# Kernel optimization log

Hardware: AMD Instinct MI355X
Metric: run time of the kernel (lower is better)

## Reference

```python
import jax, jax.numpy as jnp
import numpy as np

T_SCALE = 160
NUM_SAMPLE = 32
FEAT_DIM = 2048
HIDDEN = 512
N_CLASS = 20
BATCH = 8


def build_sample_mask(tscale=T_SCALE, ns=NUM_SAMPLE):
    # Vectorized version of _get_interp1d_mask (prop_boundary_ratio=0, num_sample_perbin=1).
    # Returns mask of shape [tscale, ns, start, end] (already transposed as in the torch code).
    s = np.arange(tscale)[:, None, None]           # start
    e = np.arange(tscale)[None, :, None]           # end
    k = np.arange(ns)[None, None, :]
    pos = s + (e - s) * k / (ns - 1.0)             # [T, T, ns] sample positions
    Sg, Eg, Kg = np.broadcast_arrays(s, e, k)
    posf = pos.ravel(); Sf = Sg.ravel(); Ef = Eg.ravel(); Kf = Kg.ravel()
    valid = Ef >= Sf
    frac, dn = np.modf(posf)
    dn = dn.astype(np.int64)
    up = np.ceil(posf).astype(np.int64)
    mask = np.zeros((tscale, ns, tscale, tscale), dtype=np.float32)
    m1 = valid & (dn >= 0) & (dn <= tscale - 1)
    np.add.at(mask, (dn[m1], Kf[m1], Sf[m1], Ef[m1]), (1.0 - frac[m1]).astype(np.float32))
    m2 = valid & (up >= 0) & (up <= tscale - 1)
    np.add.at(mask, (up[m2], Kf[m2], Sf[m2], Ef[m2]), frac[m2].astype(np.float32))
    return jnp.asarray(mask)


def conv1d(x, w, padding):
    # x: [B, Cin, T], w: [Cout, Cin, K]
    return jax.lax.conv_general_dilated(
        x, w, window_strides=(1,), padding=[(padding, padding)],
        dimension_numbers=("NCH", "OIH", "NCH"))


def setup_inputs() -> dict:
    key = jax.random.key(0)
    ks = jax.random.split(key, 6)
    x = jax.random.normal(ks[0], (BATCH, T_SCALE, FEAT_DIM), dtype=jnp.float32)
    w1 = jax.random.normal(ks[1], (HIDDEN, FEAT_DIM, 3), dtype=jnp.float32) * 0.02
    b1 = jnp.zeros((HIDDEN,), dtype=jnp.float32)
    wc = jax.random.normal(ks[2], (N_CLASS, HIDDEN, 1), dtype=jnp.float32) * 0.05
    wa = jax.random.normal(ks[3], (1, HIDDEN, 3), dtype=jnp.float32) * 0.05
    ba = jnp.zeros((1,), dtype=jnp.float32)
    sample_mask = build_sample_mask()  # [T, ns, T, T]
    return {"x": x, "sample_mask": sample_mask, "w1": w1, "b1": b1,
            "wc": wc, "wa": wa, "ba": ba}


def reference(x, sample_mask, w1, b1, wc, wa, ba):
    ns = NUM_SAMPLE
    q = ns // 4  # 8
    xp = jnp.transpose(x, (0, 2, 1))                   # [B, F, T]
    feat = jax.nn.relu(conv1d(xp, w1, 1) + b1[None, :, None])   # [B, H, T] (dropout = eval/identity)
    y_class = conv1d(feat, wc, 0)                      # [B, C, T]
    y_atn = conv1d(feat, wa, 1) + ba[None, :, None]    # [B, 1, T]
    # boundary matching: matmul against sparse interpolation mask
    out = jnp.einsum("bct,tkij->bckij", y_class, sample_mask)   # [B, C, ns, T, T]
    out_start = out[:, :, :q].mean(axis=2)
    out_mid = out[:, :, q:ns - q].mean(axis=2)
    out_end = out[:, :, ns - q:].mean(axis=2)
    bmn_class = jnp.concatenate((out_start, out_mid, out_end), axis=1)  # [B, 3C, T, T]
    sig = jax.nn.sigmoid(y_atn)
    x_fg = (sig * feat).sum(-1, keepdims=True) / (sig.sum(-1, keepdims=True) + 1e-8)  # [B, H, 1]
    y_fg = jnp.einsum("oh,bht->bot", wc[:, :, 0], x_fg)  # conv_class 1x1, no bias
    return (y_class, y_fg, bmn_class)
```

## Files before the change

kernel.cpp:

```cpp
#include <hip/hip_runtime.h>
#include <math.h>

#define TS 160
#define FEATD 2048
#define HID 512
#define NC 20
#define NB 8

typedef __attribute__((ext_vector_type(8))) short bfrag;
typedef __attribute__((ext_vector_type(4))) float f32x4;

static __device__ __forceinline__ unsigned short f2bf(float f) {
  unsigned int u = __float_as_uint(f);
  unsigned int r = (u + 0x7FFFu + ((u >> 16) & 1u)) >> 16;
  return (unsigned short)r;
}
static __device__ __forceinline__ float bf2f(unsigned short s) {
  return __uint_as_float(((unsigned int)s) << 16);
}

static __device__ __forceinline__ void gload16(const void* g, void* l) {
  __builtin_amdgcn_global_load_lds((const __attribute__((address_space(1))) void*)g,
                                   (__attribute__((address_space(3))) void*)l, 16, 0, 0);
}

__global__ __launch_bounds__(256) void k_prep(const float* __restrict__ x,
                                              const float* __restrict__ w1,
                                              unsigned short* __restrict__ xb,
                                              unsigned short* __restrict__ wb,
                                              unsigned short* __restrict__ WT) {
  __shared__ float Ls[FEATD * 3];
  const int tid = threadIdx.x;
  const int bx = blockIdx.x;
  if (bx < 1296) {
    const int idx = bx * 256 + tid;
    const int c = (idx & 255) * 8;
    const int row = idx >> 8;
    const int b = row / 162, pr = row - b * 162;
    unsigned short* o = xb + (size_t)row * FEATD + c;
    if (pr == 0 || pr == 161) {
      *(uint4*)o = make_uint4(0u, 0u, 0u, 0u);
    } else {
      const float* src = x + ((size_t)(b * TS + pr - 1)) * FEATD + c;
      float4 v0 = *(const float4*)src;
      float4 v1 = *(const float4*)(src + 4);
      unsigned short r[8] = {f2bf(v0.x), f2bf(v0.y), f2bf(v0.z), f2bf(v0.w),
                             f2bf(v1.x), f2bf(v1.y), f2bf(v1.z), f2bf(v1.w)};
      *(uint4*)o = *(const uint4*)r;
    }
  } else if (bx < 1808) {
    const int h = bx - 1296;
    const float4* src = (const float4*)(w1 + (size_t)h * (FEATD * 3));
    for (int e = tid; e < FEATD * 3 / 4; e += 256) ((float4*)Ls)[e] = src[e];
    __syncthreads();
    for (int oc = tid; oc < 768; oc += 256) {
      const int tap = oc >> 8;
      const int f0 = (oc & 255) * 8;
      unsigned short r[8];
      #pragma unroll
      for (int i = 0; i < 8; ++i) r[i] = f2bf(Ls[(f0 + i) * 3 + tap]);
      *(uint4*)&wb[((size_t)tap * HID + h) * FEATD + f0] = *(const uint4*)r;
    }
  } else {
    const int idx = (bx - 1808) * 256 + tid;
    const int tau = idx % 160;
    const int dd = (idx / 160) % 320;
    const int g = idx / (160 * 320);
    float w = 0.f;
    if (dd >= 160) {
      const int d = dd - 160;
      const int k0 = (g == 0) ? 0 : (g == 1 ? 8 : 24);
      const int k1 = (g == 0) ? 8 : (g == 1 ? 24 : 32);
      for (int k = k0; k < k1; ++k) {
        float p = (float)(d * k) / 31.0f;
        float a = fabsf(p - (float)tau);
        w += fmaxf(0.f, 1.f - a);
      }
      w *= (g == 1) ? 0.0625f : 0.125f;
    }
    WT[idx] = f2bf(w);
  }
}

__global__ __launch_bounds__(256, 3) void k_conv_mfma(const unsigned short* __restrict__ xb,
                                                      const unsigned short* __restrict__ wb,
                                                      unsigned short* __restrict__ part) {
  const int bb = blockIdx.x;
  const int h0 = blockIdx.y * 64;
  const int kz = blockIdx.z;
  const int tid = threadIdx.x;
  const int wid = tid >> 6, lane = tid & 63;

  __shared__ unsigned short Alds[162 * 64];
  __shared__ unsigned short Blds[3 * 64 * 64];

  const unsigned short* xbb = xb + (size_t)bb * 162 * FEATD;
  const unsigned short* wbb = wb + (size_t)h0 * FEATD;

  f32x4 acc[5][2] = {};
  const int wr = wid >> 1, wc = wid & 1;

  for (int s = 0; s < 4; ++s) {
    const int f0 = kz * 256 + s * 64;
    #pragma unroll
    for (int is = 0; is < 5; ++is) {
      const int ci = is * 256 + wid * 64 + lane;
      const int row = ci >> 3, c = ci & 7;
      gload16(xbb + (size_t)row * FEATD + f0 + ((c ^ (row & 7)) << 3),
              (char*)Alds + (size_t)(is * 256 + wid * 64) * 16);
    }
    #pragma unroll
    for (int is = 0; is < 6; ++is) {
      const int ci = is * 256 + wid * 64 + lane;
      const int tap = ci >> 9, rr = (ci >> 3) & 63, c = ci & 7;
      gload16(wbb + (size_t)tap * (HID * FEATD) + (size_t)rr * FEATD + f0 + ((c ^ (rr & 7)) << 3),
              (char*)Blds + (size_t)(is * 256 + wid * 64) * 16);
    }
    if (tid < 16) {
      const int row = 160 + (tid >> 3), c = tid & 7;
      uint4 v = *(const uint4*)(xbb + (size_t)row * FEATD + f0 + ((c ^ (row & 7)) << 3));
      *(uint4*)((char*)Alds + row * 128 + c * 16) = v;
    }
    __syncthreads();

    #pragma unroll
    for (int tap = 0; tap < 3; ++tap) {
      #pragma unroll
      for (int kk = 0; kk < 2; ++kk) {
        const int cread = kk * 4 + (lane >> 4);
        bfrag bf0, bf1;
        {
          const int hh0 = wc * 32 + (lane & 15);
          const int hh1 = hh0 + 16;
          bf0 = *(const bfrag*)((char*)Blds + tap * 8192 + hh0 * 128 + ((cread ^ (hh0 & 7)) << 4));
          bf1 = *(const bfrag*)((char*)Blds + tap * 8192 + hh1 * 128 + ((cread ^ (hh1 & 7)) << 4));
        }
        #pragma unroll
        for (int mi = 0; mi < 5; ++mi) {
          const int rr = wr * 80 + mi * 16 + (lane & 15) + tap;
          bfrag af = *(const bfrag*)((char*)Alds + rr * 128 + ((cread ^ (rr & 7)) << 4));
          acc[mi][0] = __builtin_amdgcn_mfma_f32_16x16x32_bf16(af, bf0, acc[mi][0], 0, 0, 0);
          acc[mi][1] = __builtin_amdgcn_mfma_f32_16x16x32_bf16(af, bf1, acc[mi][1], 0, 0, 0);
        }
      }
    }
    __syncthreads();
  }

  unsigned short* pout = part + (size_t)kz * (NB * TS) * HID;
  #pragma unroll
  for (int mi = 0; mi < 5; ++mi) {
    const int r0 = bb * TS + wr * 80 + mi * 16 + (lane >> 4) * 4;
    #pragma unroll
    for (int ni = 0; ni < 2; ++ni) {
      const int c0 = h0 + wc * 32 + ni * 16 + (lane & 15);
      #pragma unroll
      for (int i = 0; i < 4; ++i)
        pout[(size_t)(r0 + i) * HID + c0] = f2bf(acc[mi][ni][i]);
    }
  }
}

__global__ __launch_bounds__(256) void k_bias_relu(const unsigned short* __restrict__ part,
                                                   const float* __restrict__ bias,
                                                   float* __restrict__ feat) {
  const int idx = blockIdx.x * 256 + threadIdx.x;
  const int h0 = (idx & 63) * 8;
  float a[8];
  {
    float4 b0 = *(const float4*)&bias[h0];
    float4 b1 = *(const float4*)&bias[h0 + 4];
    a[0] = b0.x; a[1] = b0.y; a[2] = b0.z; a[3] = b0.w;
    a[4] = b1.x; a[5] = b1.y; a[6] = b1.z; a[7] = b1.w;
  }
  #pragma unroll
  for (int kz = 0; kz < 8; ++kz) {
    uint4 v = *(const uint4*)&part[(size_t)kz * (NB * TS * HID) + (size_t)idx * 8];
    const unsigned short* s = (const unsigned short*)&v;
    #pragma unroll
    for (int k = 0; k < 8; ++k) a[k] += bf2f(s[k]);
  }
  float4 o0, o1;
  o0.x = fmaxf(a[0], 0.f); o0.y = fmaxf(a[1], 0.f); o0.z = fmaxf(a[2], 0.f); o0.w = fmaxf(a[3], 0.f);
  o1.x = fmaxf(a[4], 0.f); o1.y = fmaxf(a[5], 0.f); o1.z = fmaxf(a[6], 0.f); o1.w = fmaxf(a[7], 0.f);
  *(float4*)&feat[(size_t)idx * 8] = o0;
  *(float4*)&feat[(size_t)idx * 8 + 4] = o1;
}

__global__ __launch_bounds__(256) void k_head(const float* __restrict__ feat,
                                              const float* __restrict__ wc,
                                              const float* __restrict__ wa,
                                              const float* __restrict__ ba,
                                              float* __restrict__ y_class,
                                              float* __restrict__ y_atn) {
  __shared__ float wcs[NC * HID];
  __shared__ float was[HID * 3];
  const int tid = threadIdx.x;
  for (int e = tid; e < NC * HID; e += 256) wcs[e] = wc[e];
  for (int e = tid; e < HID * 3; e += 256) was[e] = wa[e];
  __syncthreads();
  const int wave = blockIdx.x * 4 + (tid >> 6);
  const int lane = tid & 63;
  const int b = wave / TS, t = wave - b * TS;
  const float* frow = &feat[((size_t)b * TS + t) * HID];
  float fc[8], fm[8], fp[8];
  #pragma unroll
  for (int i2 = 0; i2 < 8; ++i2) {
    int h = lane + 64 * i2;
    fc[i2] = frow[h];
    fm[i2] = (t > 0)      ? frow[h - HID] : 0.f;
    fp[i2] = (t < TS - 1) ? frow[h + HID] : 0.f;
  }
  #pragma unroll 4
  for (int c = 0; c < NC; ++c) {
    float p = 0.f;
    #pragma unroll
    for (int i2 = 0; i2 < 8; ++i2) p += fc[i2] * wcs[c * HID + lane + 64 * i2];
    #pragma unroll
    for (int off = 32; off; off >>= 1) p += __shfl_xor(p, off);
    if (lane == 0) y_class[((size_t)b * NC + c) * TS + t] = p;
  }
  float p = 0.f;
  #pragma unroll
  for (int i2 = 0; i2 < 8; ++i2) {
    int h = lane + 64 * i2;
    p += fm[i2] * was[h * 3 + 0] + fc[i2] * was[h * 3 + 1] + fp[i2] * was[h * 3 + 2];
  }
  #pragma unroll
  for (int off = 32; off; off >>= 1) p += __shfl_xor(p, off);
  if (lane == 0) y_atn[b * TS + t] = p + ba[0];
}

__global__ __launch_bounds__(256) void k_tail(const float* __restrict__ y_class,
                                              const unsigned short* __restrict__ WT,
                                              const float* __restrict__ feat,
                                              const float* __restrict__ y_atn,
                                              const float* __restrict__ wc,
                                              float* __restrict__ y_fg,
                                              float* __restrict__ bmn) {
  __shared__ char Tlds[64000 + 65536];
  const int tid = threadIdx.x;

  if (blockIdx.y == 3) {
    if (blockIdx.x >= 8) return;
    const int b = blockIdx.x;
    float* sig = (float*)Tlds;
    float* red = sig + TS;
    float* xfg = red + 8;
    float s = 0.f;
    if (tid < TS) { s = 1.f / (1.f + expf(-y_atn[b * TS + tid])); sig[tid] = s; }
    float r = s;
    #pragma unroll
    for (int off = 32; off; off >>= 1) r += __shfl_xor(r, off);
    if ((tid & 63) == 0) red[tid >> 6] = r;
    __syncthreads();
    const float inv = 1.f / (red[0] + red[1] + red[2] + red[3] + 1e-8f);
    for (int h = tid; h < HID; h += 256) {
      float a = 0.f;
      for (int t = 0; t < TS; ++t) a += sig[t] * feat[((size_t)b * TS + t) * HID + h];
      xfg[h] = a * inv;
    }
    __syncthreads();
    const int wv = tid >> 6, lane = tid & 63;
    for (int c = wv; c < NC; c += 4) {
      float p = 0.f;
      #pragma unroll
      for (int i2 = 0; i2 < 8; ++i2) {
        int h = lane + 64 * i2;
        p += wc[c * HID + h] * xfg[h];
      }
      #pragma unroll
      for (int off = 32; off; off >>= 1) p += __shfl_xor(p, off);
      if (lane == 0) y_fg[b * NC + c] = p;
    }
    return;
  }

  char* Alds = Tlds;
  char* Wlds = Tlds + 64000;
  const int i = blockIdx.x;
  const int g = blockIdx.y;
  const int wid = tid >> 6, lane = tid & 63;

  const char* wtb = (const char*)WT + (size_t)g * 102400 + (size_t)(160 - i) * 320;
  #pragma unroll
  for (int it = 0; it < 16; ++it) {
    const int idx = it * 256 + tid;
    int row = idx / 25, c = idx - row * 25;
    if (row > 159) row = 159;
    if (c > 19) c = 0;
    gload16(wtb + (size_t)row * 320 + c * 16, Wlds + (size_t)idx * 16);
  }
  for (int e = 0; e < 13; ++e) {
    const int ci = e * 256 + tid;
    if (ci < 3200) {
      const int row = ci / 20, c = ci - row * 20;
      const int tb = i + c * 8;
      const float* yr = y_class + (size_t)row * TS;
      unsigned short r8[8];
      #pragma unroll
      for (int k = 0; k < 8; ++k) {
        const int t = tb + k;
        r8[k] = (t < TS) ? f2bf(yr[t]) : (unsigned short)0;
      }
      *(uint4*)(Alds + (size_t)row * 400 + c * 16) = *(const uint4*)r8;
    }
  }
  __syncthreads();

  const int wr = wid >> 1, wcq = wid & 1;
  f32x4 acc[5][5] = {};

  #pragma unroll
  for (int ks = 0; ks < 5; ++ks) {
    const int cc = ks * 4 + (lane >> 4);
    bfrag bfr[5];
    #pragma unroll
    for (int nf = 0; nf < 5; ++nf) {
      const int j = wcq * 80 + nf * 16 + (lane & 15);
      bfr[nf] = *(const bfrag*)(Wlds + (size_t)j * 400 + cc * 16);
    }
    #pragma unroll
    for (int mf = 0; mf < 5; ++mf) {
      const int r = wr * 80 + mf * 16 + (lane & 15);
      bfrag af = *(const bfrag*)(Alds + (size_t)r * 400 + cc * 16);
      #pragma unroll
      for (int nf = 0; nf < 5; ++nf)
        acc[mf][nf] = __builtin_amdgcn_mfma_f32_16x16x32_bf16(af, bfr[nf], acc[mf][nf], 0, 0, 0);
    }
  }

  #pragma unroll
  for (int mf = 0; mf < 5; ++mf) {
    const int r0 = wr * 80 + mf * 16 + (lane >> 4) * 4;
    #pragma unroll
    for (int reg = 0; reg < 4; ++reg) {
      const int r = r0 + reg;
      const int b = r / 20, c = r - b * 20;
      float* base = bmn + (((size_t)(b * 60 + g * 20 + c) * TS) + i) * TS;
      #pragma unroll
      for (int nf = 0; nf < 5; ++nf) {
        const int j = wcq * 80 + nf * 16 + (lane & 15);
        base[j] = acc[mf][nf][reg];
      }
    }
  }
}

extern "C" void kernel_launch(void* const* d_in, const int* in_sizes, int n_in,
                              void* d_out, int out_size, void* d_ws, size_t ws_size,
                              hipStream_t stream) {
  const float* x  = (const float*)d_in[0];
  const float* w1 = (const float*)d_in[2];
  const float* b1 = (const float*)d_in[3];
  const float* wc = (const float*)d_in[4];
  const float* wa = (const float*)d_in[5];
  const float* ba = (const float*)d_in[6];

  float* out     = (float*)d_out;
  float* y_class = out;
  float* y_fg    = out + NB * NC * TS;
  float* bmn     = out + NB * NC * TS + NB * NC;

  unsigned short* part = (unsigned short*)d_ws;
  float* feat  = (float*)((char*)d_ws + (size_t)8 * NB * TS * HID * 2);
  float* y_atn = feat + NB * TS * HID;
  unsigned short* xb = (unsigned short*)(y_atn + 2048);
  unsigned short* wb = xb + (size_t)NB * 162 * FEATD;
  unsigned short* WT = wb + (size_t)3 * HID * FEATD;

  k_prep<<<1808 + 600, 256, 0, stream>>>(x, w1, xb, wb, WT);
  k_conv_mfma<<<dim3(8, 8, 8), 256, 0, stream>>>(xb, wb, part);
  k_bias_relu<<<320, 256, 0, stream>>>(part, b1, feat);
  k_head<<<320, 256, 0, stream>>>(feat, wc, wa, ba, y_class, y_atn);
  k_tail<<<dim3(160, 4), 256, 0, stream>>>(y_class, WT, feat, y_atn, wc, y_fg, bmn);
}
```

Baseline: 76.08 us.

## Widen conv tile to 128 channels, double split-K, fuse bias-relu with head

Each conv block now computes a 128-wide hidden tile instead of 64 and split-K goes from 8 to 16 slices, so the weight tile gets more reuse per A load. The bias+ReLU reduction and the classifier/attention head are merged into one kernel with one block per (batch,time) row. The 3-tap attention conv is computed by scattering per-row partial sums with atomics into y_atn, which k_prep pre-initialises to the bias. Costs are twice as many bf16 partial buffers to write and read, lower occupancy from the larger accumulator and LDS tile, and float-atomic ordering nondeterminism.

```diff
diff --git a/kernel.cpp b/kernel.cpp
--- a/kernel.cpp
+++ b/kernel.cpp
@@ -6,6 +6,7 @@
 #define HID 512
 #define NC 20
 #define NB 8
+#define KZ 16
 
 typedef __attribute__((ext_vector_type(8))) short bfrag;
 typedef __attribute__((ext_vector_type(4))) float f32x4;
@@ -26,9 +27,11 @@
 
 __global__ __launch_bounds__(256) void k_prep(const float* __restrict__ x,
                                               const float* __restrict__ w1,
+                                              const float* __restrict__ ba,
                                               unsigned short* __restrict__ xb,
                                               unsigned short* __restrict__ wb,
-                                              unsigned short* __restrict__ WT) {
+                                              unsigned short* __restrict__ WT,
+                                              float* __restrict__ y_atn) {
   __shared__ float Ls[FEATD * 3];
   const int tid = threadIdx.x;
   const int bx = blockIdx.x;
@@ -61,7 +64,7 @@
       for (int i = 0; i < 8; ++i) r[i] = f2bf(Ls[(f0 + i) * 3 + tap]);
       *(uint4*)&wb[((size_t)tap * HID + h) * FEATD + f0] = *(const uint4*)r;
     }
-  } else {
+  } else if (bx < 2408) {
     const int idx = (bx - 1808) * 256 + tid;
     const int tau = idx % 160;
     const int dd = (idx / 160) % 320;
@@ -79,29 +82,31 @@
       w *= (g == 1) ? 0.0625f : 0.125f;
     }
     WT[idx] = f2bf(w);
-  }
-}
-
-__global__ __launch_bounds__(256, 3) void k_conv_mfma(const unsigned short* __restrict__ xb,
+  } else {
+    const int idx = (bx - 2408) * 256 + tid;
+    if (idx < NB * TS) y_atn[idx] = ba[0];
+  }
+}
+
+__global__ __launch_bounds__(256, 2) void k_conv_mfma(const unsigned short* __restrict__ xb,
                                                       const unsigned short* __restrict__ wb,
                                                       unsigned short* __restrict__ part) {
   const int bb = blockIdx.x;
-  const int h0 = blockIdx.y * 64;
+  const int hq = blockIdx.y;
   const int kz = blockIdx.z;
   const int tid = threadIdx.x;
   const int wid = tid >> 6, lane = tid & 63;
 
   __shared__ unsigned short Alds[162 * 64];
-  __shared__ unsigned short Blds[3 * 64 * 64];
+  __shared__ unsigned short Blds[3 * 128 * 64];
 
   const unsigned short* xbb = xb + (size_t)bb * 162 * FEATD;
-  const unsigned short* wbb = wb + (size_t)h0 * FEATD;
-
-  f32x4 acc[5][2] = {};
+
+  f32x4 acc[5][4] = {};
   const int wr = wid >> 1, wc = wid & 1;
 
-  for (int s = 0; s < 4; ++s) {
-    const int f0 = kz * 256 + s * 64;
+  for (int s = 0; s < 2; ++s) {
+    const int f0 = kz * 128 + s * 64;
     #pragma unroll
     for (int is = 0; is < 5; ++is) {
       const int ci = is * 256 + wid * 64 + lane;
@@ -110,10 +115,10 @@
               (char*)Alds + (size_t)(is * 256 + wid * 64) * 16);
     }
     #pragma unroll
-    for (int is = 0; is < 6; ++is) {
+    for (int is = 0; is < 12; ++is) {
       const int ci = is * 256 + wid * 64 + lane;
-      const int tap = ci >> 9, rr = (ci >> 3) & 63, c = ci & 7;
-      gload16(wbb + (size_t)tap * (HID * FEATD) + (size_t)rr * FEATD + f0 + ((c ^ (rr & 7)) << 3),
+      const int tap = ci >> 10, rr = (ci >> 3) & 127, c = ci & 7;
+      gload16(wb + ((size_t)(tap * HID + hq * 128 + rr)) * FEATD + f0 + ((c ^ (rr & 7)) << 3),
               (char*)Blds + (size_t)(is * 256 + wid * 64) * 16);
     }
     if (tid < 16) {
@@ -127,20 +132,20 @@
     for (int tap = 0; tap < 3; ++tap) {
       #pragma unroll
       for (int kk = 0; kk < 2; ++kk) {
-        const int cread = kk * 4 + (lane >> 4);
-        bfrag bf0, bf1;
-        {
-          const int hh0 = wc * 32 + (lane & 15);
-          const int hh1 = hh0 + 16;
-          bf0 = *(const bfrag*)((char*)Blds + tap * 8192 + hh0 * 128 + ((cread ^ (hh0 & 7)) << 4));
-          bf1 = *(const bfrag*)((char*)Blds + tap * 8192 + hh1 * 128 + ((cread ^ (hh1 & 7)) << 4));
+        const int cc = kk * 4 + (lane >> 4);
+        bfrag bfr[4];
+        #pragma unroll
+        for (int nf = 0; nf < 4; ++nf) {
+          const int hh = wc * 64 + nf * 16 + (lane & 15);
+          bfr[nf] = *(const bfrag*)((char*)Blds + (size_t)(((tap * 128 + hh) * 8) + (cc ^ (hh & 7))) * 16);
         }
         #pragma unroll
         for (int mi = 0; mi < 5; ++mi) {
           const int rr = wr * 80 + mi * 16 + (lane & 15) + tap;
-          bfrag af = *(const bfrag*)((char*)Alds + rr * 128 + ((cread ^ (rr & 7)) << 4));
-          acc[mi][0] = __builtin_amdgcn_mfma_f32_16x16x32_bf16(af, bf0, acc[mi][0], 0, 0, 0);
-          acc[mi][1] = __builtin_amdgcn_mfma_f32_16x16x32_bf16(af, bf1, acc[mi][1], 0, 0, 0);
+          bfrag af = *(const bfrag*)((char*)Alds + (size_t)((rr * 8) + (cc ^ (rr & 7))) * 16);
+          #pragma unroll
+          for (int nf = 0; nf < 4; ++nf)
+            acc[mi][nf] = __builtin_amdgcn_mfma_f32_16x16x32_bf16(af, bfr[nf], acc[mi][nf], 0, 0, 0);
         }
       }
     }
@@ -152,83 +157,68 @@
   for (int mi = 0; mi < 5; ++mi) {
     const int r0 = bb * TS + wr * 80 + mi * 16 + (lane >> 4) * 4;
     #pragma unroll
-    for (int ni = 0; ni < 2; ++ni) {
-      const int c0 = h0 + wc * 32 + ni * 16 + (lane & 15);
+    for (int nf = 0; nf < 4; ++nf) {
+      const int c0 = hq * 128 + wc * 64 + nf * 16 + (lane & 15);
       #pragma unroll
       for (int i = 0; i < 4; ++i)
-        pout[(size_t)(r0 + i) * HID + c0] = f2bf(acc[mi][ni][i]);
-    }
-  }
-}
-
-__global__ __launch_bounds__(256) void k_bias_relu(const unsigned short* __restrict__ part,
-                                                   const float* __restrict__ bias,
-                                                   float* __restrict__ feat) {
-  const int idx = blockIdx.x * 256 + threadIdx.x;
-  const int h0 = (idx & 63) * 8;
-  float a[8];
-  {
-    float4 b0 = *(const float4*)&bias[h0];
-    float4 b1 = *(const float4*)&bias[h0 + 4];
-    a[0] = b0.x; a[1] = b0.y; a[2] = b0.z; a[3] = b0.w;
-    a[4] = b1.x; a[5] = b1.y; a[6] = b1.z; a[7] = b1.w;
-  }
-  #pragma unroll
-  for (int kz = 0; kz < 8; ++kz) {
-    uint4 v = *(const uint4*)&part[(size_t)kz * (NB * TS * HID) + (size_t)idx * 8];
-    const unsigned short* s = (const unsigned short*)&v;
-    #pragma unroll
-    for (int k = 0; k < 8; ++k) a[k] += bf2f(s[k]);
-  }
-  float4 o0, o1;
-  o0.x = fmaxf(a[0], 0.f); o0.y = fmaxf(a[1], 0.f); o0.z = fmaxf(a[2], 0.f); o0.w = fmaxf(a[3], 0.f);
-  o1.x = fmaxf(a[4], 0.f); o1.y = fmaxf(a[5], 0.f); o1.z = fmaxf(a[6], 0.f); o1.w = fmaxf(a[7], 0.f);
-  *(float4*)&feat[(size_t)idx * 8] = o0;
-  *(float4*)&feat[(size_t)idx * 8 + 4] = o1;
-}
-
-__global__ __launch_bounds__(256) void k_head(const float* __restrict__ feat,
-                                              const float* __restrict__ wc,
-                                              const float* __restrict__ wa,
-                                              const float* __restrict__ ba,
-                                              float* __restrict__ y_class,
-                                              float* __restrict__ y_atn) {
-  __shared__ float wcs[NC * HID];
-  __shared__ float was[HID * 3];
+        pout[(size_t)(r0 + i) * HID + c0] = f2bf(acc[mi][nf][i]);
+    }
+  }
+}
+
+__global__ __launch_bounds__(256) void k_feat_head(const unsigned short* __restrict__ part,
+                                                   const float* __restrict__ b1,
+                                                   const float* __restrict__ wc,
+                                                   const float* __restrict__ wa,
+                                                   float* __restrict__ feat,
+                                                   float* __restrict__ y_class,
+                                                   float* __restrict__ y_atn) {
+  const int bt = blockIdx.x;
   const int tid = threadIdx.x;
-  for (int e = tid; e < NC * HID; e += 256) wcs[e] = wc[e];
-  for (int e = tid; e < HID * 3; e += 256) was[e] = wa[e];
+  __shared__ float fr[HID];
+  __shared__ float sred[4][3];
+  const int h0 = tid * 2;
+  float a0 = b1[h0], a1 = b1[h0 + 1];
+  #pragma unroll
+  for (int kz = 0; kz < KZ; ++kz) {
+    unsigned int v = *(const unsigned int*)&part[(size_t)kz * (NB * TS * HID) + (size_t)bt * HID + h0];
+    a0 += bf2f((unsigned short)(v & 0xffff));
+    a1 += bf2f((unsigned short)(v >> 16));
+  }
+  a0 = fmaxf(a0, 0.f);
+  a1 = fmaxf(a1, 0.f);
+  float2 fo; fo.x = a0; fo.y = a1;
+  *(float2*)&feat[(size_t)bt * HID + h0] = fo;
+  fr[h0] = a0; fr[h0 + 1] = a1;
+  float s0 = a0 * wa[h0 * 3 + 0] + a1 * wa[h0 * 3 + 3];
+  float s1 = a0 * wa[h0 * 3 + 1] + a1 * wa[h0 * 3 + 4];
+  float s2 = a0 * wa[h0 * 3 + 2] + a1 * wa[h0 * 3 + 5];
+  #pragma unroll
+  for (int off = 32; off; off >>= 1) {
+    s0 += __shfl_xor(s0, off);
+    s1 += __shfl_xor(s1, off);
+    s2 += __shfl_xor(s2, off);
+  }
+  const int wv = tid >> 6, lane = tid & 63;
+  if (lane == 0) { sred[wv][0] = s0; sred[wv][1] = s1; sred[wv][2] = s2; }
   __syncthreads();
-  const int wave = blockIdx.x * 4 + (tid >> 6);
-  const int lane = tid & 63;
-  const int b = wave / TS, t = wave - b * TS;
-  const float* frow = &feat[((size_t)b * TS + t) * HID];
-  float fc[8], fm[8], fp[8];
-  #pragma unroll
-  for (int i2 = 0; i2 < 8; ++i2) {
-    int h = lane + 64 * i2;
-    fc[i2] = frow[h];
-    fm[i2] = (t > 0)      ? frow[h - HID] : 0.f;
-    fp[i2] = (t < TS - 1) ? frow[h + HID] : 0.f;
-  }
-  #pragma unroll 4
-  for (int c = 0; c < NC; ++c) {
+  const int b = bt / TS, t = bt - b * TS;
+  for (int c = wv; c < NC; c += 4) {
     float p = 0.f;
     #pragma unroll
-    for (int i2 = 0; i2 < 8; ++i2) p += fc[i2] * wcs[c * HID + lane + 64 * i2];
+    for (int i2 = 0; i2 < 8; ++i2) p += fr[lane + 64 * i2] * wc[c * HID + lane + 64 * i2];
     #pragma unroll
     for (int off = 32; off; off >>= 1) p += __shfl_xor(p, off);
     if (lane == 0) y_class[((size_t)b * NC + c) * TS + t] = p;
   }
-  float p = 0.f;
-  #pragma unroll
-  for (int i2 = 0; i2 < 8; ++i2) {
-    int h = lane + 64 * i2;
-    p += fm[i2] * was[h * 3 + 0] + fc[i2] * was[h * 3 + 1] + fp[i2] * was[h * 3 + 2];
-  }
-  #pragma unroll
-  for (int off = 32; off; off >>= 1) p += __shfl_xor(p, off);
-  if (lane == 0) y_atn[b * TS + t] = p + ba[0];
+  if (tid == 0) {
+    float S0 = sred[0][0] + sred[1][0] + sred[2][0] + sred[3][0];
+    float S1 = sred[0][1] + sred[1][1] + sred[2][1] + sred[3][1];
+    float S2 = sred[0][2] + sred[1][2] + sred[2][2] + sred[3][2];
+    atomicAdd(&y_atn[bt], S1);
+    if (t < TS - 1) atomicAdd(&y_atn[bt + 1], S0);
+    if (t > 0)      atomicAdd(&y_atn[bt - 1], S2);
+  }
 }
 
 __global__ __launch_bounds__(256) void k_tail(const float* __restrict__ y_class,
@@ -242,7 +232,7 @@
   const int tid = threadIdx.x;
 
   if (blockIdx.y == 3) {
-    if (blockIdx.x >= 8) return;
+    if (blockIdx.x >= NB) return;
     const int b = blockIdx.x;
     float* sig = (float*)Tlds;
     float* red = sig + TS;
@@ -363,15 +353,14 @@
   float* bmn     = out + NB * NC * TS + NB * NC;
 
   unsigned short* part = (unsigned short*)d_ws;
-  float* feat  = (float*)((char*)d_ws + (size_t)8 * NB * TS * HID * 2);
+  float* feat  = (float*)((char*)d_ws + (size_t)KZ * NB * TS * HID * 2);
   float* y_atn = feat + NB * TS * HID;
   unsigned short* xb = (unsigned short*)(y_atn + 2048);
   unsigned short* wb = xb + (size_t)NB * 162 * FEATD;
   unsigned short* WT = wb + (size_t)3 * HID * FEATD;
 
-  k_prep<<<1808 + 600, 256, 0, stream>>>(x, w1, xb, wb, WT);
-  k_conv_mfma<<<dim3(8, 8, 8), 256, 0, stream>>>(xb, wb, part);
-  k_bias_relu<<<320, 256, 0, stream>>>(part, b1, feat);
-  k_head<<<320, 256, 0, stream>>>(feat, wc, wa, ba, y_class, y_atn);
+  k_prep<<<2413, 256, 0, stream>>>(x, w1, ba, xb, wb, WT, y_atn);
+  k_conv_mfma<<<dim3(8, 4, KZ), 256, 0, stream>>>(xb, wb, part);
+  k_feat_head<<<NB * TS, 256, 0, stream>>>(part, b1, wc, wa, feat, y_class, y_atn);
   k_tail<<<dim3(160, 4), 256, 0, stream>>>(y_class, WT, feat, y_atn, wc, y_fg, bmn);
 }
```

Result: faster. 72.38 us (-4.9%).
